# Kernel tuning notes

Measured on AMD Instinct MI355X. Metric: run time of the kernel, lower is better.

The kernel has to match this reference:

```python
import jax, jax.numpy as jnp
import numpy as np

H = 16
DK = 64


def setup_inputs() -> dict:
    key = jax.random.key(0)
    ks = jax.random.split(key, 10)
    dps, seq_len, d = 32, 2048, 1024
    xavier = float(np.sqrt(2.0 / (DK + DK)))  # xavier_normal_ for square dk x dk
    return {
        "S": jax.random.normal(ks[0], (dps, seq_len, d), dtype=jnp.float32),
        "R": jax.random.normal(ks[1], (dps, 1, d), dtype=jnp.float32),
        "S_mas": jax.random.randint(ks[2], (dps, seq_len, 1), 0, 2, dtype=jnp.int32),
        "R_mas": jax.random.randint(ks[3], (dps, 1, 1), 0, 2, dtype=jnp.int32),
        "WQ_w": jax.random.normal(ks[4], (DK, DK), dtype=jnp.float32) * xavier,
        "WQ_b": jnp.zeros((DK,), dtype=jnp.float32),
        "WK_w": jax.random.normal(ks[5], (DK, DK), dtype=jnp.float32) * xavier,
        "WK_b": jnp.zeros((DK,), dtype=jnp.float32),
        "WV_w": jax.random.normal(ks[6], (DK, DK), dtype=jnp.float32) * xavier,
        "WV_b": jnp.zeros((DK,), dtype=jnp.float32),
    }


def reference(S, R, S_mas, R_mas, WQ_w, WQ_b, WK_w, WK_b, WV_w, WV_b):
    dps, seq_len, d = S.shape
    # split heads: (dps, seq, h, dk) -- permute-free since projections are per last dim
    S4 = S.reshape(dps, seq_len, H, DK)
    R4 = R.reshape(dps, 1, H, DK)
    # only S_Q, R_K, R_V affect the output (S_K, S_V, R_Q are dead in the original)
    S_Q = jnp.einsum("bshd,ed->bshe", S4, WQ_w) + WQ_b
    R_K = jnp.einsum("bshd,ed->bshe", R4, WK_w) + WK_b  # (dps,1,h,dk)
    R_V = jnp.einsum("bshd,ed->bshe", R4, WV_w) + WV_b  # (dps,1,h,dk)
    # dot-product gate per (batch, token, head)
    beta = jnp.sum(S_Q * R_K, axis=-1, keepdims=True)  # (dps,seq,h,1)
    S_Z = R_V * beta                                   # (dps,seq,h,dk)
    mask = (S_mas != 0)[:, :, :, None]                 # (dps,seq,1,1)
    S_Z = jnp.where(mask, S_Z, 0.0)
    return S_Z.reshape(dps, seq_len, H * DK)
```

## Files before the change

### kernel.cpp

```cpp
#include <hip/hip_runtime.h>

#define H 16
#define DK 64

typedef float vfloat4 __attribute__((ext_vector_type(4)));

__global__ __launch_bounds__(64) void prep_kernel(
    const float* __restrict__ R,
    const float* __restrict__ WQ_w, const float* __restrict__ WQ_b,
    const float* __restrict__ WK_w, const float* __restrict__ WK_b,
    const float* __restrict__ WV_w, const float* __restrict__ WV_b,
    float* __restrict__ u, float* __restrict__ rv, float* __restrict__ c) {
    const int bh = blockIdx.x;
    const int e  = threadIdx.x;
    __shared__ float r_s[DK];
    __shared__ float rk_s[DK];

    r_s[e] = R[bh * DK + e];
    __syncthreads();

    float rk  = WK_b[e];
    float rvv = WV_b[e];
#pragma unroll
    for (int d = 0; d < DK; ++d) {
        rk  += r_s[d] * WK_w[e * DK + d];
        rvv += r_s[d] * WV_w[e * DK + d];
    }
    rk_s[e] = rk;
    rv[bh * DK + e] = rvv;
    __syncthreads();

    float uu = 0.f;
#pragma unroll
    for (int ee = 0; ee < DK; ++ee) uu += WQ_w[ee * DK + e] * rk_s[ee];
    u[bh * DK + e] = uu;

    if (e == 0) {
        float cc = 0.f;
        for (int ee = 0; ee < DK; ++ee) cc += WQ_b[ee] * rk_s[ee];
        c[bh] = cc;
    }
}

#define ROWS_PER_BLOCK 16

__global__ __launch_bounds__(256) void fused_kernel(
    const float* __restrict__ S, const int* __restrict__ S_mas,
    const float* __restrict__ u, const float* __restrict__ rv,
    const float* __restrict__ c, float* __restrict__ out,
    int seq_len, int blocks_per_batch) {
    const int t = threadIdx.x;
    const int h = t >> 4;
    const int b = blockIdx.x / blocks_per_batch;
    const int srow0 = (blockIdx.x % blocks_per_batch) * ROWS_PER_BLOCK;
    const int d_model = H * DK;

    const int bh = b * H + h;
    const vfloat4 u4  = *(const vfloat4*)(u  + bh * DK + (t & 15) * 4);
    const vfloat4 rv4 = *(const vfloat4*)(rv + bh * DK + (t & 15) * 4);
    const float   ch  = c[bh];

    const size_t base = (size_t)b * seq_len * d_model + (size_t)srow0 * d_model + t * 4;
    const float* srow = S + base;
    float*       orow = out + base;
    const int*   mrow = S_mas + (size_t)b * seq_len + srow0;

    int m[ROWS_PER_BLOCK];
#pragma unroll
    for (int r = 0; r < ROWS_PER_BLOCK; ++r) m[r] = mrow[r];

    vfloat4 sdat[ROWS_PER_BLOCK];
#pragma unroll
    for (int r = 0; r < ROWS_PER_BLOCK; ++r) {
        const size_t off = (m[r] != 0) ? (size_t)r * d_model : 0;
        sdat[r] = *(const vfloat4*)(srow + off);
    }

#pragma unroll
    for (int r = 0; r < ROWS_PER_BLOCK; ++r) {
        const vfloat4 s4 = sdat[r];
        float p = s4.x * u4.x + s4.y * u4.y + s4.z * u4.z + s4.w * u4.w;
        p += __shfl_xor(p, 1);
        p += __shfl_xor(p, 2);
        p += __shfl_xor(p, 4);
        p += __shfl_xor(p, 8);
        const float beta = p + ch;
        vfloat4 o4;
        const bool live = (m[r] != 0);
        o4.x = live ? rv4.x * beta : 0.f;
        o4.y = live ? rv4.y * beta : 0.f;
        o4.z = live ? rv4.z * beta : 0.f;
        o4.w = live ? rv4.w * beta : 0.f;
        __builtin_nontemporal_store(o4, (vfloat4*)(orow + (size_t)r * d_model));
    }
}

extern "C" void kernel_launch(void* const* d_in, const int* in_sizes, int n_in,
                              void* d_out, int out_size, void* d_ws, size_t ws_size,
                              hipStream_t stream) {
    const float* S     = (const float*)d_in[0];
    const float* R     = (const float*)d_in[1];
    const int*   S_mas = (const int*)d_in[2];
    const float* WQ_w  = (const float*)d_in[4];
    const float* WQ_b  = (const float*)d_in[5];
    const float* WK_w  = (const float*)d_in[6];
    const float* WK_b  = (const float*)d_in[7];
    const float* WV_w  = (const float*)d_in[8];
    const float* WV_b  = (const float*)d_in[9];
    float* out = (float*)d_out;

    const int d_model = H * DK;
    const int dps     = in_sizes[1] / d_model;
    const int seq_len = in_sizes[0] / (dps * d_model);

    float* u_ws  = (float*)d_ws;
    float* rv_ws = u_ws + (size_t)dps * H * DK;
    float* c_ws  = rv_ws + (size_t)dps * H * DK;

    prep_kernel<<<dps * H, 64, 0, stream>>>(R, WQ_w, WQ_b, WK_w, WK_b, WV_w, WV_b,
                                            u_ws, rv_ws, c_ws);

    const int blocks_per_batch = seq_len / ROWS_PER_BLOCK;
    fused_kernel<<<dps * blocks_per_batch, 256, 0, stream>>>(
        S, S_mas, u_ws, rv_ws, c_ws, out, seq_len, blocks_per_batch);
}
```

Measured before the change: 439.0 us.

## Double-buffer row tiles in fused kernel with scalar mask branching

Each block now processes 64 rows in 8-row tiles, using two register buffers so the loads for the next tile are issued while the current tile is computed and stored. Mask values are staged in shared memory and made wave-uniform with readfirstlane, so loads of masked-out rows are skipped entirely instead of redirected to row 0. Launch bounds now request 4 blocks per SM, and the grid shrinks because each block covers more rows. The aim is to overlap memory latency and cut read traffic for masked rows, at the cost of fewer blocks and a shared-memory sync.

```diff
diff --git a/kernel.cpp b/kernel.cpp
--- a/kernel.cpp
+++ b/kernel.cpp
@@ -42,57 +42,80 @@
     }
 }
 
-#define ROWS_PER_BLOCK 16
+#define TILE 8
+#define TILES_PER_BLOCK 8
+#define ROWS_PER_BLOCK (TILE * TILES_PER_BLOCK)
 
-__global__ __launch_bounds__(256) void fused_kernel(
+#define ISSUE(BUF, TL)                                                        \
+    do {                                                                      \
+        _Pragma("unroll")                                                     \
+        for (int r = 0; r < TILE; ++r) {                                      \
+            const int mm =                                                    \
+                __builtin_amdgcn_readfirstlane(msh[(TL) * TILE + r]);         \
+            if (mm)                                                           \
+                BUF[r] = *(const vfloat4*)(sbase +                            \
+                                           (size_t)((TL) * TILE + r) * 1024); \
+            else                                                              \
+                BUF[r] = (vfloat4)(0.f);                                      \
+        }                                                                     \
+    } while (0)
+
+#define COMPUTE(BUF, TL)                                                      \
+    do {                                                                      \
+        _Pragma("unroll")                                                     \
+        for (int r = 0; r < TILE; ++r) {                                      \
+            const vfloat4 s4 = BUF[r];                                        \
+            float p = s4.x * u4.x + s4.y * u4.y + s4.z * u4.z + s4.w * u4.w;  \
+            p += __shfl_xor(p, 1);                                            \
+            p += __shfl_xor(p, 2);                                            \
+            p += __shfl_xor(p, 4);                                            \
+            p += __shfl_xor(p, 8);                                            \
+            const float beta = p + ch;                                        \
+            const int mm = msh[(TL) * TILE + r];                              \
+            vfloat4 o4;                                                       \
+            o4.x = mm ? rv4.x * beta : 0.f;                                   \
+            o4.y = mm ? rv4.y * beta : 0.f;                                   \
+            o4.z = mm ? rv4.z * beta : 0.f;                                   \
+            o4.w = mm ? rv4.w * beta : 0.f;                                   \
+            __builtin_nontemporal_store(                                      \
+                o4, (vfloat4*)(obase + (size_t)((TL) * TILE + r) * 1024));    \
+        }                                                                     \
+    } while (0)
+
+__global__ __launch_bounds__(256, 4) void fused_kernel(
     const float* __restrict__ S, const int* __restrict__ S_mas,
     const float* __restrict__ u, const float* __restrict__ rv,
     const float* __restrict__ c, float* __restrict__ out,
     int seq_len, int blocks_per_batch) {
     const int t = threadIdx.x;
-    const int h = t >> 4;
     const int b = blockIdx.x / blocks_per_batch;
-    const int srow0 = (blockIdx.x % blocks_per_batch) * ROWS_PER_BLOCK;
+    const int row0 = (blockIdx.x % blocks_per_batch) * ROWS_PER_BLOCK;
     const int d_model = H * DK;
 
-    const int bh = b * H + h;
+    const int bh = b * H + (t >> 4);
     const vfloat4 u4  = *(const vfloat4*)(u  + bh * DK + (t & 15) * 4);
     const vfloat4 rv4 = *(const vfloat4*)(rv + bh * DK + (t & 15) * 4);
     const float   ch  = c[bh];
 
-    const size_t base = (size_t)b * seq_len * d_model + (size_t)srow0 * d_model + t * 4;
-    const float* srow = S + base;
-    float*       orow = out + base;
-    const int*   mrow = S_mas + (size_t)b * seq_len + srow0;
+    const size_t base = (size_t)b * seq_len * d_model + (size_t)row0 * d_model + t * 4;
+    const float* sbase = S + base;
+    float*       obase = out + base;
 
-    int m[ROWS_PER_BLOCK];
-#pragma unroll
-    for (int r = 0; r < ROWS_PER_BLOCK; ++r) m[r] = mrow[r];
+    __shared__ int msh[ROWS_PER_BLOCK];
+    if (t < ROWS_PER_BLOCK) msh[t] = S_mas[(size_t)b * seq_len + row0 + t];
+    __syncthreads();
 
-    vfloat4 sdat[ROWS_PER_BLOCK];
-#pragma unroll
-    for (int r = 0; r < ROWS_PER_BLOCK; ++r) {
-        const size_t off = (m[r] != 0) ? (size_t)r * d_model : 0;
-        sdat[r] = *(const vfloat4*)(srow + off);
-    }
+    vfloat4 A[TILE], B[TILE];
 
-#pragma unroll
-    for (int r = 0; r < ROWS_PER_BLOCK; ++r) {
-        const vfloat4 s4 = sdat[r];
-        float p = s4.x * u4.x + s4.y * u4.y + s4.z * u4.z + s4.w * u4.w;
-        p += __shfl_xor(p, 1);
-        p += __shfl_xor(p, 2);
-        p += __shfl_xor(p, 4);
-        p += __shfl_xor(p, 8);
-        const float beta = p + ch;
-        vfloat4 o4;
-        const bool live = (m[r] != 0);
-        o4.x = live ? rv4.x * beta : 0.f;
-        o4.y = live ? rv4.y * beta : 0.f;
-        o4.z = live ? rv4.z * beta : 0.f;
-        o4.w = live ? rv4.w * beta : 0.f;
-        __builtin_nontemporal_store(o4, (vfloat4*)(orow + (size_t)r * d_model));
-    }
+    ISSUE(A, 0);
+    ISSUE(B, 1); COMPUTE(A, 0);
+    ISSUE(A, 2); COMPUTE(B, 1);
+    ISSUE(B, 3); COMPUTE(A, 2);
+    ISSUE(A, 4); COMPUTE(B, 3);
+    ISSUE(B, 5); COMPUTE(A, 4);
+    ISSUE(A, 6); COMPUTE(B, 5);
+    ISSUE(B, 7); COMPUTE(A, 6);
+    COMPUTE(B, 7);
 }
 
 extern "C" void kernel_launch(void* const* d_in, const int* in_sizes, int n_in,
```

New measurement: 511.4 us. 16.5% more time.
